# Kernel optimization log

Measured on AMD Instinct MI355X. Metric: run time of the kernel, lower is better.

## Reference

```python
import jax, jax.numpy as jnp
import numpy as np
from jax import lax

T, N, E = 12, 10000, 160000
C_IN, C_H, C_OUT = 32, 64, 32
EPS = 1e-5


def _glorot(key, shape):
    fan_in, fan_out = shape[-2] if len(shape) > 1 else shape[0], shape[-1]
    s = (6.0 / (fan_in + fan_out)) ** 0.5
    return jax.random.uniform(key, shape, jnp.float32, -s, s)


def setup_inputs() -> dict:
    key = jax.random.key(0)
    ks = jax.random.split(key, 16)
    inp = {
        "x": jax.random.normal(ks[0], (T, N, C_IN), jnp.float32),
        "edge_index": jax.random.randint(ks[1], (2, E), 0, N, jnp.int32),
        "edge_weight": jax.random.uniform(ks[2], (E,), jnp.float32),
        # layer 1 (input layer): in=C_IN -> C_H
        "conv_w1": _glorot(ks[3], (C_H, C_IN, 3)) * 0.1,
        "conv_b1": jnp.zeros((C_H,), jnp.float32),
        "gamma1": jnp.ones((C_H,), jnp.float32),
        "beta1": jnp.zeros((C_H,), jnp.float32),
        "gcn_w1": _glorot(ks[4], (C_H, C_H)),
        "gcn_b1": jnp.zeros((C_H,), jnp.float32),
        # layer 2 (hidden layer): C_H -> C_H
        "conv_w2": _glorot(ks[5], (C_H, C_H, 3)) * 0.1,
        "conv_b2": jnp.zeros((C_H,), jnp.float32),
        "gamma2": jnp.ones((C_H,), jnp.float32),
        "beta2": jnp.zeros((C_H,), jnp.float32),
        "gcn_w2": _glorot(ks[6], (C_H, C_H)),
        "gcn_b2": jnp.zeros((C_H,), jnp.float32),
        # output linear: C_H -> C_OUT
        "out_w": _glorot(ks[7], (C_H, C_OUT)),
        "out_b": jnp.zeros((C_OUT,), jnp.float32),
    }
    return inp


def _stgcn_layer(x, edge_index, edge_weight, cw, cb, gamma, beta, gw, gb):
    # x: [T, N, C_in]  ->  torch.stack(x).permute(1,2,0) = [N, C_in, T]
    xs = jnp.transpose(x, (1, 2, 0))
    h = lax.conv_general_dilated(xs, cw, (1,), [(1, 1)],
                                 dimension_numbers=("NCH", "OIH", "NCH"))
    h = h + cb[None, :, None]
    # InstanceNorm1d(affine) over the temporal dim
    mu = h.mean(-1, keepdims=True)
    var = ((h - mu) ** 2).mean(-1, keepdims=True)
    h = (h - mu) * lax.rsqrt(var + EPS) * gamma[None, :, None] + beta[None, :, None]
    h = jax.nn.relu(h)
    h = jnp.transpose(h, (2, 0, 1))  # [T, N, C_out]
    # GCNConv per timestep (vectorized over T)
    src, dst = edge_index[0], edge_index[1]
    n = h.shape[1]
    deg = jnp.zeros((n,), h.dtype).at[dst].add(edge_weight) + 1.0  # self-loop weight 1
    dis = lax.rsqrt(deg)
    norm = dis[src] * edge_weight * dis[dst]  # [E]
    xw = jnp.einsum("tnc,cd->tnd", h, gw)  # [T, N, C_out]
    msg = xw[:, src, :] * norm[None, :, None]  # [T, E, C_out]
    agg = jax.vmap(lambda m: jax.ops.segment_sum(m, dst, num_segments=n))(msg)
    agg = agg + (dis * dis)[None, :, None] * xw + gb  # self loop + bias
    return agg


def reference(x, edge_index, edge_weight,
              conv_w1, conv_b1, gamma1, beta1, gcn_w1, gcn_b1,
              conv_w2, conv_b2, gamma2, beta2, gcn_w2, gcn_b2,
              out_w, out_b):
    h = _stgcn_layer(x, edge_index, edge_weight,
                     conv_w1, conv_b1, gamma1, beta1, gcn_w1, gcn_b1)
    h = _stgcn_layer(h, edge_index, edge_weight,
                     conv_w2, conv_b2, gamma2, beta2, gcn_w2, gcn_b2)
    out = jnp.einsum("tnc,co->tno", h, out_w) + out_b  # per-t linear
    return out.mean(axis=0)  # [N, C_OUT]
```

## Files before the change

kernel.cpp:

```cpp
#include <hip/hip_runtime.h>
#include <hip/hip_bf16.h>
#include <stdint.h>

#define MAXDEG 64

typedef short s16x8 __attribute__((ext_vector_type(8)));
typedef short s16x4 __attribute__((ext_vector_type(4)));
typedef float f32x4 __attribute__((ext_vector_type(4)));

static __device__ __forceinline__ float us2f(unsigned short u) {
    union { float f; unsigned int i; } cv; cv.i = ((unsigned int)u) << 16; return cv.f;
}
static __device__ __forceinline__ unsigned short f2us(float f) {
    __hip_bfloat16 h = __float2bfloat16(f);
    return *(unsigned short*)&h;
}

__global__ void k_build_ell(const int* __restrict__ ei, const float* __restrict__ ew,
                            float* __restrict__ deg, unsigned* __restrict__ cnt,
                            int2* __restrict__ ell, int E)
{
    int e = blockIdx.x * 256 + threadIdx.x;
    if (e >= E) return;
    int s = ei[e], d = ei[E + e];
    float w = ew[e];
    atomicAdd(&deg[d], w);
    unsigned slot = atomicAdd(&cnt[d], 1u);
    if (slot < MAXDEG) ell[(size_t)d * MAXDEG + slot] = make_int2(s, __float_as_int(w));
}

__global__ void k_norm(int2* __restrict__ ell, const unsigned* __restrict__ cnt,
                       const float* __restrict__ deg, int N)
{
    int idx = blockIdx.x * 256 + threadIdx.x;
    if (idx >= N * MAXDEG) return;
    int n = idx >> 6;
    int s = idx & (MAXDEG - 1);
    unsigned dg = cnt[n]; if (dg > MAXDEG) dg = MAXDEG;
    if ((unsigned)s >= dg) return;
    int2 p = ell[idx];
    unsigned sx = (unsigned)p.x;
    float nrm = (sx < (unsigned)N)
        ? rsqrtf(deg[sx] + 1.0f) * __int_as_float(p.y) * rsqrtf(deg[n] + 1.0f) : 0.f;
    ell[idx] = make_int2(p.x, __float_as_int(nrm));
}

#define ACCE(NRM, V0, V1, V2)                                                          \
    a[0] = fmaf(NRM, us2f(V0.x), a[0]);  a[1] = fmaf(NRM, us2f(V0.y), a[1]);           \
    a[2] = fmaf(NRM, us2f(V0.z), a[2]);  a[3] = fmaf(NRM, us2f(V0.w), a[3]);           \
    a[4] = fmaf(NRM, us2f(V1.x), a[4]);  a[5] = fmaf(NRM, us2f(V1.y), a[5]);           \
    a[6] = fmaf(NRM, us2f(V1.z), a[6]);  a[7] = fmaf(NRM, us2f(V1.w), a[7]);           \
    a[8] = fmaf(NRM, us2f(V2.x), a[8]);  a[9] = fmaf(NRM, us2f(V2.y), a[9]);           \
    a[10] = fmaf(NRM, us2f(V2.z), a[10]); a[11] = fmaf(NRM, us2f(V2.w), a[11]);

#define EDGE_GATHER(P)                                                      \
    {                                                                       \
        unsigned sx = (unsigned)(P).x;                                      \
        if (sx >= (unsigned)N) sx = 0;          \
        float nrm = __int_as_float((P).y);                                  \
        const unsigned short* qp = xw_in + (size_t)sx * 768 + L * 4;        \
        ushort4 w0 = *(const ushort4*)qp;                                   \
        ushort4 w1 = *(const ushort4*)(qp + 256);                           \
        ushort4 w2 = *(const ushort4*)(qp + 512);                           \
        ACCE(nrm, w0, w1, w2)                                               \
    }

template<int CIN>
__global__ __launch_bounds__(512, 4) void k_layer_a(
    const float* __restrict__ x_in,
    const float* __restrict__ cw,
    const float* __restrict__ gm, const float* __restrict__ bt,
    const float* __restrict__ gw,
    unsigned short* __restrict__ xw_out, int N)
{
    constexpr int KT   = CIN / 32;
    constexpr int WSTR = (CIN == 64) ? 72 : 40;
    __shared__ __align__(16) short WT[3 * 64 * WSTR];
    __shared__ __align__(16) short gwT[64 * 72];
    __shared__ __align__(16) short xh[8][14 * 72];

    const int tid = threadIdx.x;
    const int nn = tid >> 6;
    const int c = tid & 63;
    const int m = c & 15;
    const int q = c >> 4;
    const int mrow = (m < 12) ? m : 11;
    int n = blockIdx.x * 8 + nn;
    if (n >= N) n = N - 1;

    for (int g = tid; g < 3 * 64 * CIN; g += 512) {
        int kk = g / (64 * CIN);
        int r = g - kk * 64 * CIN;
        int cc = r / CIN, ci = r - cc * CIN;
        WT[kk * (64 * WSTR) + cc * WSTR + ci] = (short)f2us(cw[(cc * CIN + ci) * 3 + kk]);
    }
    for (int g = tid; g < 4096; g += 512) {
        int cc = g >> 6, d = g & 63;
        gwT[d * 72 + cc] = (short)f2us(gw[g]);
    }
    #pragma unroll
    for (int it = 0; it < (12 * CIN) / 64; ++it) {
        int i = it * 64 + c;
        int t = i / CIN, ci = i - t * CIN;
        xh[nn][(t + 1) * 72 + ci] = (short)f2us(x_in[((size_t)t * N + n) * CIN + ci]);
    }
    if (c < CIN) { xh[nn][c] = 0; xh[nn][13 * 72 + c] = 0; }
    __syncthreads();

    f32x4 acc[4];
    #pragma unroll
    for (int nt = 0; nt < 4; ++nt) acc[nt] = (f32x4){0.f, 0.f, 0.f, 0.f};
    #pragma unroll
    for (int kk = 0; kk < 3; ++kk) {
        #pragma unroll
        for (int kt = 0; kt < KT; ++kt) {
            s16x8 aA = *(const s16x8*)&xh[nn][(mrow + kk) * 72 + kt * 32 + q * 8];
            #pragma unroll
            for (int nt = 0; nt < 4; ++nt) {
                s16x8 bB = *(const s16x8*)&WT[kk * (64 * WSTR) + (nt * 16 + m) * WSTR + kt * 32 + q * 8];
                acc[nt] = __builtin_amdgcn_mfma_f32_16x16x32_bf16(aA, bB, acc[nt], 0, 0, 0);
            }
        }
    }

    #pragma unroll
    for (int nt = 0; nt < 4; ++nt) {
        float s  = acc[nt][0] + acc[nt][1] + acc[nt][2] + acc[nt][3];
        float s2 = acc[nt][0] * acc[nt][0] + acc[nt][1] * acc[nt][1]
                 + acc[nt][2] * acc[nt][2] + acc[nt][3] * acc[nt][3];
        if (q == 3) { s = 0.f; s2 = 0.f; }
        s  += __shfl_xor(s, 16);  s  += __shfl_xor(s, 32);
        s2 += __shfl_xor(s2, 16); s2 += __shfl_xor(s2, 32);
        const float mu  = s * (1.f / 12.f);
        const float var = s2 * (1.f / 12.f) - mu * mu;
        const float scn = rsqrtf(var + 1e-5f) * gm[nt * 16 + m];
        const float sbn = bt[nt * 16 + m];
        if (q < 3) {
            #pragma unroll
            for (int reg = 0; reg < 4; ++reg) {
                float h = fmaf(acc[nt][reg] - mu, scn, sbn);
                h = h > 0.f ? h : 0.f;
                xh[nn][(q * 4 + reg) * 72 + nt * 16 + m] = (short)f2us(h);
            }
        }
    }

    s16x8 a2[2];
    #pragma unroll
    for (int kt2 = 0; kt2 < 2; ++kt2)
        a2[kt2] = *(const s16x8*)&xh[nn][mrow * 72 + kt2 * 32 + q * 8];
    f32x4 acc2[4];
    #pragma unroll
    for (int nt = 0; nt < 4; ++nt) acc2[nt] = (f32x4){0.f, 0.f, 0.f, 0.f};
    #pragma unroll
    for (int nt = 0; nt < 4; ++nt) {
        #pragma unroll
        for (int kt2 = 0; kt2 < 2; ++kt2) {
            s16x8 b2 = *(const s16x8*)&gwT[(nt * 16 + m) * 72 + kt2 * 32 + q * 8];
            acc2[nt] = __builtin_amdgcn_mfma_f32_16x16x32_bf16(a2[kt2], b2, acc2[nt], 0, 0, 0);
        }
    }

    unsigned short* dst = xw_out + (size_t)n * 768;
    if (q < 3) {
        #pragma unroll
        for (int nt = 0; nt < 4; ++nt)
            #pragma unroll
            for (int reg = 0; reg < 4; ++reg)
                dst[(q * 4 + reg) * 64 + nt * 16 + m] = f2us(acc2[nt][reg]);
    }
}

__global__ __launch_bounds__(512, 4) void k_gather_a(
    const unsigned short* __restrict__ xw_in,
    const int2* __restrict__ ell, const unsigned* __restrict__ cnt,
    const float* __restrict__ deg, const float* __restrict__ gb,
    const float* __restrict__ cw,
    const float* __restrict__ gm, const float* __restrict__ bt,
    const float* __restrict__ gw,
    unsigned short* __restrict__ rowmean, int N)
{
    constexpr int WSTR = 72;
    __shared__ __align__(16) short WT[3 * 64 * WSTR];
    __shared__ __align__(16) short gwT[64 * 72];
    __shared__ __align__(16) short xh[8][14 * 72];

    const int tid = threadIdx.x;
    const int nn = tid >> 6;
    const int L = tid & 63;
    const int m = L & 15;
    const int q = L >> 4;
    const int mrow = (m < 12) ? m : 11;
    int n = blockIdx.x * 8 + nn;
    if (n >= N) n = N - 1;

    for (int g = tid; g < 3 * 64 * 64; g += 512) {
        int kk = g >> 12;
        int r = g & 4095;
        int cc = r >> 6, ci = r & 63;
        WT[kk * (64 * WSTR) + cc * WSTR + ci] = (short)f2us(cw[(cc * 64 + ci) * 3 + kk]);
    }
    for (int g = tid; g < 4096; g += 512) {
        int cc = g >> 6, d = g & 63;
        gwT[d * 72 + cc] = (short)f2us(gw[g]);
    }
    xh[nn][L] = 0; xh[nn][13 * 72 + L] = 0;
    __syncthreads();

    const float dn = rsqrtf(deg[n] + 1.0f);
    const float d2 = dn * dn;
    float a[12];
    {
        const unsigned short* self = xw_in + (size_t)n * 768 + L * 4;
        ushort4 v0 = *(const ushort4*)self;
        ushort4 v1 = *(const ushort4*)(self + 256);
        ushort4 v2 = *(const ushort4*)(self + 512);
        const int c0 = (L * 4) & 63;
        const float g0 = gb[c0], g1 = gb[c0 + 1], g2 = gb[c0 + 2], g3 = gb[c0 + 3];
        a[0] = fmaf(d2, us2f(v0.x), g0); a[1] = fmaf(d2, us2f(v0.y), g1);
        a[2] = fmaf(d2, us2f(v0.z), g2); a[3] = fmaf(d2, us2f(v0.w), g3);
        a[4] = fmaf(d2, us2f(v1.x), g0); a[5] = fmaf(d2, us2f(v1.y), g1);
        a[6] = fmaf(d2, us2f(v1.z), g2); a[7] = fmaf(d2, us2f(v1.w), g3);
        a[8] = fmaf(d2, us2f(v2.x), g0); a[9] = fmaf(d2, us2f(v2.y), g1);
        a[10] = fmaf(d2, us2f(v2.z), g2); a[11] = fmaf(d2, us2f(v2.w), g3);
    }
    unsigned dg = cnt[n]; if (dg > MAXDEG) dg = MAXDEG;
    const int2* row = ell + (size_t)n * MAXDEG;
    unsigned e = 0;
    for (; e + 4 <= dg; e += 4) {
        int2 p0 = row[e], p1 = row[e + 1], p2 = row[e + 2], p3 = row[e + 3];
        EDGE_GATHER(p0) EDGE_GATHER(p1) EDGE_GATHER(p2) EDGE_GATHER(p3)
    }
    for (; e < dg; ++e) { int2 p0 = row[e]; EDGE_GATHER(p0) }

    #pragma unroll
    for (int j = 0; j < 3; ++j) {
        s16x4 s4 = { (short)f2us(a[j * 4 + 0]), (short)f2us(a[j * 4 + 1]),
                     (short)f2us(a[j * 4 + 2]), (short)f2us(a[j * 4 + 3]) };
        *(s16x4*)&xh[nn][(j * 4 + q + 1) * 72 + ((L * 4) & 63)] = s4;
    }

    f32x4 acc[4];
    #pragma unroll
    for (int nt = 0; nt < 4; ++nt) acc[nt] = (f32x4){0.f, 0.f, 0.f, 0.f};
    #pragma unroll
    for (int kk = 0; kk < 3; ++kk) {
        #pragma unroll
        for (int kt = 0; kt < 2; ++kt) {
            s16x8 aA = *(const s16x8*)&xh[nn][(mrow + kk) * 72 + kt * 32 + q * 8];
            #pragma unroll
            for (int nt = 0; nt < 4; ++nt) {
                s16x8 bB = *(const s16x8*)&WT[kk * (64 * WSTR) + (nt * 16 + m) * WSTR + kt * 32 + q * 8];
                acc[nt] = __builtin_amdgcn_mfma_f32_16x16x32_bf16(aA, bB, acc[nt], 0, 0, 0);
            }
        }
    }

    #pragma unroll
    for (int nt = 0; nt < 4; ++nt) {
        float s  = acc[nt][0] + acc[nt][1] + acc[nt][2] + acc[nt][3];
        float s2 = acc[nt][0] * acc[nt][0] + acc[nt][1] * acc[nt][1]
                 + acc[nt][2] * acc[nt][2] + acc[nt][3] * acc[nt][3];
        if (q == 3) { s = 0.f; s2 = 0.f; }
        s  += __shfl_xor(s, 16);  s  += __shfl_xor(s, 32);
        s2 += __shfl_xor(s2, 16); s2 += __shfl_xor(s2, 32);
        const float mu  = s * (1.f / 12.f);
        const float var = s2 * (1.f / 12.f) - mu * mu;
        const float scn = rsqrtf(var + 1e-5f) * gm[nt * 16 + m];
        const float sbn = bt[nt * 16 + m];
        if (q < 3) {
            #pragma unroll
            for (int reg = 0; reg < 4; ++reg) {
                float h = fmaf(acc[nt][reg] - mu, scn, sbn);
                h = h > 0.f ? h : 0.f;
                xh[nn][(q * 4 + reg) * 72 + nt * 16 + m] = (short)f2us(h);
            }
        }
    }

    s16x8 a2[2];
    #pragma unroll
    for (int kt2 = 0; kt2 < 2; ++kt2)
        a2[kt2] = *(const s16x8*)&xh[nn][mrow * 72 + kt2 * 32 + q * 8];
    f32x4 acc2[4];
    #pragma unroll
    for (int nt = 0; nt < 4; ++nt) acc2[nt] = (f32x4){0.f, 0.f, 0.f, 0.f};
    #pragma unroll
    for (int nt = 0; nt < 4; ++nt) {
        #pragma unroll
        for (int kt2 = 0; kt2 < 2; ++kt2) {
            s16x8 b2 = *(const s16x8*)&gwT[(nt * 16 + m) * 72 + kt2 * 32 + q * 8];
            acc2[nt] = __builtin_amdgcn_mfma_f32_16x16x32_bf16(a2[kt2], b2, acc2[nt], 0, 0, 0);
        }
    }

    #pragma unroll
    for (int nt = 0; nt < 4; ++nt) {
        float pm = (q < 3) ? (acc2[nt][0] + acc2[nt][1] + acc2[nt][2] + acc2[nt][3]) : 0.f;
        pm += __shfl_xor(pm, 16); pm += __shfl_xor(pm, 32);
        if (q == 0)
            rowmean[(size_t)n * 64 + nt * 16 + m] = f2us(pm * (1.f / 12.f));
    }
}

__global__ __launch_bounds__(256) void k_final(
    const unsigned short* __restrict__ rowmean, const int2* __restrict__ ell,
    const unsigned* __restrict__ cnt, const float* __restrict__ deg,
    const float* __restrict__ gb,
    const float* __restrict__ ow, const float* __restrict__ ob,
    float* __restrict__ dout, int N)
{
    __shared__ __align__(16) float hbuf[4][64];
    const int tid = threadIdx.x;
    const int nn = tid >> 6, L = tid & 63;
    int n = blockIdx.x * 4 + nn;
    if (n >= N) n = N - 1;
    const float dn = rsqrtf(deg[n] + 1.0f);
    const float d2 = dn * dn;

    float a = fmaf(d2, us2f(rowmean[(size_t)n * 64 + L]), gb[L]);

    unsigned dg = cnt[n]; if (dg > MAXDEG) dg = MAXDEG;
    const int2* row = ell + (size_t)n * MAXDEG;
    unsigned e = 0;
    for (; e + 8 <= dg; e += 8) {
        #pragma unroll
        for (int i = 0; i < 8; ++i) {
            int2 p = row[e + i];
            unsigned sx = (unsigned)p.x;
            if (sx >= (unsigned)N) sx = 0;
            a = fmaf(__int_as_float(p.y), us2f(rowmean[(size_t)sx * 64 + L]), a);
        }
    }
    for (; e < dg; ++e) {
        int2 p = row[e];
        unsigned sx = (unsigned)p.x;
        if (sx >= (unsigned)N) sx = 0;
        a = fmaf(__int_as_float(p.y), us2f(rowmean[(size_t)sx * 64 + L]), a);
    }

    hbuf[nn][L] = a;
    __syncthreads();
    if (L < 32) {
        float oa = ob[L];
        #pragma unroll
        for (int cc = 0; cc < 64; ++cc)
            oa = fmaf(hbuf[nn][cc], ow[cc * 32 + L], oa);
        dout[(size_t)n * 32 + L] = oa;
    }
}

extern "C" void kernel_launch(void* const* d_in, const int* in_sizes, int n_in,
                              void* d_out, int out_size, void* d_ws, size_t ws_size,
                              hipStream_t stream)
{
    const float* x   = (const float*)d_in[0];
    const int*   ei  = (const int*)d_in[1];
    const float* ew  = (const float*)d_in[2];
    const float* cw1 = (const float*)d_in[3];
    const float* gm1 = (const float*)d_in[5];
    const float* bt1 = (const float*)d_in[6];
    const float* gw1 = (const float*)d_in[7];
    const float* gb1 = (const float*)d_in[8];
    const float* cw2 = (const float*)d_in[9];
    const float* gm2 = (const float*)d_in[11];
    const float* bt2 = (const float*)d_in[12];
    const float* gw2 = (const float*)d_in[13];
    const float* gb2 = (const float*)d_in[14];
    const float* ow  = (const float*)d_in[15];
    const float* ob  = (const float*)d_in[16];

    const int N = in_sizes[0] / (12 * 32);
    const int E = in_sizes[2];

    char* p0 = (char*)d_ws;
    char* p = p0;
    float* deg = (float*)p;          p += (size_t)N * 4;
    unsigned* cnt = (unsigned*)p;    p += (size_t)N * 4;
    p = (char*)(((uintptr_t)p + 255) & ~(uintptr_t)255);
    int2* ell = (int2*)p;            p += (size_t)N * MAXDEG * 8;
    p = (char*)(((uintptr_t)p + 255) & ~(uintptr_t)255);
    unsigned short* bufXW1 = (unsigned short*)p; p += (size_t)N * 768 * 2;
    unsigned short* rowmean = (unsigned short*)p; p += (size_t)N * 64 * 2;

    const size_t need = (size_t)(p - p0);
    if (ws_size < need) {
        hipMemsetAsync(d_out, 0, (size_t)out_size * 4, stream);
        return;
    }

    hipMemsetAsync(deg, 0, (size_t)N * 8, stream);

    const int eb  = (E + 255) / 256;
    const int nb8 = (N + 7) / 8;
    const int nb4 = (N + 3) / 4;
    k_build_ell<<<eb, 256, 0, stream>>>(ei, ew, deg, cnt, ell, E);
    k_norm<<<(N * MAXDEG + 255) / 256, 256, 0, stream>>>(ell, cnt, deg, N);

    k_layer_a<32><<<nb8, 512, 0, stream>>>(x, cw1, gm1, bt1, gw1, bufXW1, N);
    k_gather_a<<<nb8, 512, 0, stream>>>(bufXW1, ell, cnt, deg, gb1,
                                        cw2, gm2, bt2, gw2, rowmean, N);
    k_final<<<nb4, 256, 0, stream>>>(rowmean, ell, cnt, deg, gb2, ow, ob, (float*)d_out, N);
}
```

Measured before the change: 194.0 us.

## Use persistent blocks with atomic work-stealing for layer and gather kernels

Converts k_layer_a and k_gather_a into persistent kernels with a fixed grid (1024 and 768 blocks). Each wavefront takes node indices from a global atomic counter and loops until all nodes are done. This amortizes the per-block staging of conv and GCN weights into shared memory over many nodes and balances the uneven per-node degree work in the gather. The cost is one atomic per node per wavefront and two counters zeroed by the existing memset.

Measured after the change: 543.3 us. +180.1%, slower.

```diff
diff --git a/kernel.cpp b/kernel.cpp
--- a/kernel.cpp
+++ b/kernel.cpp
@@ -71,7 +71,7 @@
     const float* __restrict__ cw,
     const float* __restrict__ gm, const float* __restrict__ bt,
     const float* __restrict__ gw,
-    unsigned short* __restrict__ xw_out, int N)
+    unsigned short* __restrict__ xw_out, unsigned* __restrict__ ctr, int N)
 {
     constexpr int KT   = CIN / 32;
     constexpr int WSTR = (CIN == 64) ? 72 : 40;
@@ -85,8 +85,6 @@
     const int m = c & 15;
     const int q = c >> 4;
     const int mrow = (m < 12) ? m : 11;
-    int n = blockIdx.x * 8 + nn;
-    if (n >= N) n = N - 1;
 
     for (int g = tid; g < 3 * 64 * CIN; g += 512) {
         int kk = g / (64 * CIN);
@@ -98,76 +96,85 @@
         int cc = g >> 6, d = g & 63;
         gwT[d * 72 + cc] = (short)f2us(gw[g]);
     }
-    #pragma unroll
-    for (int it = 0; it < (12 * CIN) / 64; ++it) {
-        int i = it * 64 + c;
-        int t = i / CIN, ci = i - t * CIN;
-        xh[nn][(t + 1) * 72 + ci] = (short)f2us(x_in[((size_t)t * N + n) * CIN + ci]);
-    }
-    if (c < CIN) { xh[nn][c] = 0; xh[nn][13 * 72 + c] = 0; }
+    if (c < CIN) xh[nn][13 * 72 + c] = 0;
     __syncthreads();
 
-    f32x4 acc[4];
-    #pragma unroll
-    for (int nt = 0; nt < 4; ++nt) acc[nt] = (f32x4){0.f, 0.f, 0.f, 0.f};
-    #pragma unroll
-    for (int kk = 0; kk < 3; ++kk) {
-        #pragma unroll
-        for (int kt = 0; kt < KT; ++kt) {
-            s16x8 aA = *(const s16x8*)&xh[nn][(mrow + kk) * 72 + kt * 32 + q * 8];
+    for (;;) {
+        unsigned n;
+        if (c == 0) n = atomicAdd(ctr, 1u);
+        n = (unsigned)__shfl((int)n, 0);
+        if (n >= (unsigned)N) break;
+
+        if (c < CIN) xh[nn][c] = 0;
+        #pragma unroll
+        for (int it = 0; it < (12 * CIN) / 64; ++it) {
+            int i = it * 64 + c;
+            int t = i / CIN, ci = i - t * CIN;
+            xh[nn][(t + 1) * 72 + ci] = (short)f2us(x_in[((size_t)t * N + n) * CIN + ci]);
+        }
+
+        f32x4 acc[4];
+        #pragma unroll
+        for (int nt = 0; nt < 4; ++nt) acc[nt] = (f32x4){0.f, 0.f, 0.f, 0.f};
+        #pragma unroll
+        for (int kk = 0; kk < 3; ++kk) {
             #pragma unroll
-            for (int nt = 0; nt < 4; ++nt) {
-                s16x8 bB = *(const s16x8*)&WT[kk * (64 * WSTR) + (nt * 16 + m) * WSTR + kt * 32 + q * 8];
-                acc[nt] = __builtin_amdgcn_mfma_f32_16x16x32_bf16(aA, bB, acc[nt], 0, 0, 0);
-            }
-        }
-    }
-
-    #pragma unroll
-    for (int nt = 0; nt < 4; ++nt) {
-        float s  = acc[nt][0] + acc[nt][1] + acc[nt][2] + acc[nt][3];
-        float s2 = acc[nt][0] * acc[nt][0] + acc[nt][1] * acc[nt][1]
-                 + acc[nt][2] * acc[nt][2] + acc[nt][3] * acc[nt][3];
-        if (q == 3) { s = 0.f; s2 = 0.f; }
-        s  += __shfl_xor(s, 16);  s  += __shfl_xor(s, 32);
-        s2 += __shfl_xor(s2, 16); s2 += __shfl_xor(s2, 32);
-        const float mu  = s * (1.f / 12.f);
-        const float var = s2 * (1.f / 12.f) - mu * mu;
-        const float scn = rsqrtf(var + 1e-5f) * gm[nt * 16 + m];
-        const float sbn = bt[nt * 16 + m];
+            for (int kt = 0; kt < KT; ++kt) {
+                s16x8 aA = *(const s16x8*)&xh[nn][(mrow + kk) * 72 + kt * 32 + q * 8];
+                #pragma unroll
+                for (int nt = 0; nt < 4; ++nt) {
+                    s16x8 bB = *(const s16x8*)&WT[kk * (64 * WSTR) + (nt * 16 + m) * WSTR + kt * 32 + q * 8];
+                    acc[nt] = __builtin_amdgcn_mfma_f32_16x16x32_bf16(aA, bB, acc[nt], 0, 0, 0);
+                }
+            }
+        }
+
+        #pragma unroll
+        for (int nt = 0; nt < 4; ++nt) {
+            float s  = acc[nt][0] + acc[nt][1] + acc[nt][2] + acc[nt][3];
+            float s2 = acc[nt][0] * acc[nt][0] + acc[nt][1] * acc[nt][1]
+                     + acc[nt][2] * acc[nt][2] + acc[nt][3] * acc[nt][3];
+            if (q == 3) { s = 0.f; s2 = 0.f; }
+            s  += __shfl_xor(s, 16);  s  += __shfl_xor(s, 32);
+            s2 += __shfl_xor(s2, 16); s2 += __shfl_xor(s2, 32);
+            const float mu  = s * (1.f / 12.f);
+            const float var = s2 * (1.f / 12.f) - mu * mu;
+            const float scn = rsqrtf(var + 1e-5f) * gm[nt * 16 + m];
+            const float sbn = bt[nt * 16 + m];
+            if (q < 3) {
+                #pragma unroll
+                for (int reg = 0; reg < 4; ++reg) {
+                    float h = fmaf(acc[nt][reg] - mu, scn, sbn);
+                    h = h > 0.f ? h : 0.f;
+                    xh[nn][(q * 4 + reg) * 72 + nt * 16 + m] = (short)f2us(h);
+                }
+            }
+        }
+
+        s16x8 a2[2];
+        #pragma unroll
+        for (int kt2 = 0; kt2 < 2; ++kt2)
+            a2[kt2] = *(const s16x8*)&xh[nn][mrow * 72 + kt2 * 32 + q * 8];
+        f32x4 acc2[4];
+        #pragma unroll
+        for (int nt = 0; nt < 4; ++nt) acc2[nt] = (f32x4){0.f, 0.f, 0.f, 0.f};
+        #pragma unroll
+        for (int nt = 0; nt < 4; ++nt) {
+            #pragma unroll
+            for (int kt2 = 0; kt2 < 2; ++kt2) {
+                s16x8 b2 = *(const s16x8*)&gwT[(nt * 16 + m) * 72 + kt2 * 32 + q * 8];
+                acc2[nt] = __builtin_amdgcn_mfma_f32_16x16x32_bf16(a2[kt2], b2, acc2[nt], 0, 0, 0);
+            }
+        }
+
+        unsigned short* dst = xw_out + (size_t)n * 768;
         if (q < 3) {
             #pragma unroll
-            for (int reg = 0; reg < 4; ++reg) {
-                float h = fmaf(acc[nt][reg] - mu, scn, sbn);
-                h = h > 0.f ? h : 0.f;
-                xh[nn][(q * 4 + reg) * 72 + nt * 16 + m] = (short)f2us(h);
-            }
-        }
-    }
-
-    s16x8 a2[2];
-    #pragma unroll
-    for (int kt2 = 0; kt2 < 2; ++kt2)
-        a2[kt2] = *(const s16x8*)&xh[nn][mrow * 72 + kt2 * 32 + q * 8];
-    f32x4 acc2[4];
-    #pragma unroll
-    for (int nt = 0; nt < 4; ++nt) acc2[nt] = (f32x4){0.f, 0.f, 0.f, 0.f};
-    #pragma unroll
-    for (int nt = 0; nt < 4; ++nt) {
-        #pragma unroll
-        for (int kt2 = 0; kt2 < 2; ++kt2) {
-            s16x8 b2 = *(const s16x8*)&gwT[(nt * 16 + m) * 72 + kt2 * 32 + q * 8];
-            acc2[nt] = __builtin_amdgcn_mfma_f32_16x16x32_bf16(a2[kt2], b2, acc2[nt], 0, 0, 0);
-        }
-    }
-
-    unsigned short* dst = xw_out + (size_t)n * 768;
-    if (q < 3) {
-        #pragma unroll
-        for (int nt = 0; nt < 4; ++nt)
-            #pragma unroll
-            for (int reg = 0; reg < 4; ++reg)
-                dst[(q * 4 + reg) * 64 + nt * 16 + m] = f2us(acc2[nt][reg]);
+            for (int nt = 0; nt < 4; ++nt)
+                #pragma unroll
+                for (int reg = 0; reg < 4; ++reg)
+                    dst[(q * 4 + reg) * 64 + nt * 16 + m] = f2us(acc2[nt][reg]);
+        }
     }
 }
 
@@ -178,7 +185,7 @@
     const float* __restrict__ cw,
     const float* __restrict__ gm, const float* __restrict__ bt,
     const float* __restrict__ gw,
-    unsigned short* __restrict__ rowmean, int N)
+    unsigned short* __restrict__ rowmean, unsigned* __restrict__ ctr, int N)
 {
     constexpr int WSTR = 72;
     __shared__ __align__(16) short WT[3 * 64 * WSTR];
@@ -191,8 +198,6 @@
     const int m = L & 15;
     const int q = L >> 4;
     const int mrow = (m < 12) ? m : 11;
-    int n = blockIdx.x * 8 + nn;
-    if (n >= N) n = N - 1;
 
     for (int g = tid; g < 3 * 64 * 64; g += 512) {
         int kk = g >> 12;
@@ -204,102 +209,110 @@
         int cc = g >> 6, d = g & 63;
         gwT[d * 72 + cc] = (short)f2us(gw[g]);
     }
-    xh[nn][L] = 0; xh[nn][13 * 72 + L] = 0;
+    xh[nn][13 * 72 + L] = 0;
     __syncthreads();
 
-    const float dn = rsqrtf(deg[n] + 1.0f);
-    const float d2 = dn * dn;
-    float a[12];
-    {
-        const unsigned short* self = xw_in + (size_t)n * 768 + L * 4;
-        ushort4 v0 = *(const ushort4*)self;
-        ushort4 v1 = *(const ushort4*)(self + 256);
-        ushort4 v2 = *(const ushort4*)(self + 512);
-        const int c0 = (L * 4) & 63;
-        const float g0 = gb[c0], g1 = gb[c0 + 1], g2 = gb[c0 + 2], g3 = gb[c0 + 3];
-        a[0] = fmaf(d2, us2f(v0.x), g0); a[1] = fmaf(d2, us2f(v0.y), g1);
-        a[2] = fmaf(d2, us2f(v0.z), g2); a[3] = fmaf(d2, us2f(v0.w), g3);
-        a[4] = fmaf(d2, us2f(v1.x), g0); a[5] = fmaf(d2, us2f(v1.y), g1);
-        a[6] = fmaf(d2, us2f(v1.z), g2); a[7] = fmaf(d2, us2f(v1.w), g3);
-        a[8] = fmaf(d2, us2f(v2.x), g0); a[9] = fmaf(d2, us2f(v2.y), g1);
-        a[10] = fmaf(d2, us2f(v2.z), g2); a[11] = fmaf(d2, us2f(v2.w), g3);
-    }
-    unsigned dg = cnt[n]; if (dg > MAXDEG) dg = MAXDEG;
-    const int2* row = ell + (size_t)n * MAXDEG;
-    unsigned e = 0;
-    for (; e + 4 <= dg; e += 4) {
-        int2 p0 = row[e], p1 = row[e + 1], p2 = row[e + 2], p3 = row[e + 3];
-        EDGE_GATHER(p0) EDGE_GATHER(p1) EDGE_GATHER(p2) EDGE_GATHER(p3)
-    }
-    for (; e < dg; ++e) { int2 p0 = row[e]; EDGE_GATHER(p0) }
-
-    #pragma unroll
-    for (int j = 0; j < 3; ++j) {
-        s16x4 s4 = { (short)f2us(a[j * 4 + 0]), (short)f2us(a[j * 4 + 1]),
-                     (short)f2us(a[j * 4 + 2]), (short)f2us(a[j * 4 + 3]) };
-        *(s16x4*)&xh[nn][(j * 4 + q + 1) * 72 + ((L * 4) & 63)] = s4;
-    }
-
-    f32x4 acc[4];
-    #pragma unroll
-    for (int nt = 0; nt < 4; ++nt) acc[nt] = (f32x4){0.f, 0.f, 0.f, 0.f};
-    #pragma unroll
-    for (int kk = 0; kk < 3; ++kk) {
-        #pragma unroll
-        for (int kt = 0; kt < 2; ++kt) {
-            s16x8 aA = *(const s16x8*)&xh[nn][(mrow + kk) * 72 + kt * 32 + q * 8];
+    for (;;) {
+        unsigned n;
+        if (L == 0) n = atomicAdd(ctr, 1u);
+        n = (unsigned)__shfl((int)n, 0);
+        if (n >= (unsigned)N) break;
+
+        const float dn = rsqrtf(deg[n] + 1.0f);
+        const float d2 = dn * dn;
+        float a[12];
+        {
+            const unsigned short* self = xw_in + (size_t)n * 768 + L * 4;
+            ushort4 v0 = *(const ushort4*)self;
+            ushort4 v1 = *(const ushort4*)(self + 256);
+            ushort4 v2 = *(const ushort4*)(self + 512);
+            const int c0 = (L * 4) & 63;
+            const float g0 = gb[c0], g1 = gb[c0 + 1], g2 = gb[c0 + 2], g3 = gb[c0 + 3];
+            a[0] = fmaf(d2, us2f(v0.x), g0); a[1] = fmaf(d2, us2f(v0.y), g1);
+            a[2] = fmaf(d2, us2f(v0.z), g2); a[3] = fmaf(d2, us2f(v0.w), g3);
+            a[4] = fmaf(d2, us2f(v1.x), g0); a[5] = fmaf(d2, us2f(v1.y), g1);
+            a[6] = fmaf(d2, us2f(v1.z), g2); a[7] = fmaf(d2, us2f(v1.w), g3);
+            a[8] = fmaf(d2, us2f(v2.x), g0); a[9] = fmaf(d2, us2f(v2.y), g1);
+            a[10] = fmaf(d2, us2f(v2.z), g2); a[11] = fmaf(d2, us2f(v2.w), g3);
+        }
+        unsigned dg = cnt[n]; if (dg > MAXDEG) dg = MAXDEG;
+        const int2* row = ell + (size_t)n * MAXDEG;
+        unsigned e = 0;
+        for (; e + 4 <= dg; e += 4) {
+            int2 p0 = row[e], p1 = row[e + 1], p2 = row[e + 2], p3 = row[e + 3];
+            EDGE_GATHER(p0) EDGE_GATHER(p1) EDGE_GATHER(p2) EDGE_GATHER(p3)
+        }
+        for (; e < dg; ++e) { int2 p0 = row[e]; EDGE_GATHER(p0) }
+
+        xh[nn][L] = 0;
+        #pragma unroll
+        for (int j = 0; j < 3; ++j) {
+            s16x4 s4 = { (short)f2us(a[j * 4 + 0]), (short)f2us(a[j * 4 + 1]),
+                         (short)f2us(a[j * 4 + 2]), (short)f2us(a[j * 4 + 3]) };
+            *(s16x4*)&xh[nn][(j * 4 + q + 1) * 72 + ((L * 4) & 63)] = s4;
+        }
+
+        f32x4 acc[4];
+        #pragma unroll
+        for (int nt = 0; nt < 4; ++nt) acc[nt] = (f32x4){0.f, 0.f, 0.f, 0.f};
+        #pragma unroll
+        for (int kk = 0; kk < 3; ++kk) {
             #pragma unroll
-            for (int nt = 0; nt < 4; ++nt) {
-                s16x8 bB = *(const s16x8*)&WT[kk * (64 * WSTR) + (nt * 16 + m) * WSTR + kt * 32 + q * 8];
-                acc[nt] = __builtin_amdgcn_mfma_f32_16x16x32_bf16(aA, bB, acc[nt], 0, 0, 0);
-            }
-        }
-    }
-
-    #pragma unroll
-    for (int nt = 0; nt < 4; ++nt) {
-        float s  = acc[nt][0] + acc[nt][1] + acc[nt][2] + acc[nt][3];
-        float s2 = acc[nt][0] * acc[nt][0] + acc[nt][1] * acc[nt][1]
-                 + acc[nt][2] * acc[nt][2] + acc[nt][3] * acc[nt][3];
-        if (q == 3) { s = 0.f; s2 = 0.f; }
-        s  += __shfl_xor(s, 16);  s  += __shfl_xor(s, 32);
-        s2 += __shfl_xor(s2, 16); s2 += __shfl_xor(s2, 32);
-        const float mu  = s * (1.f / 12.f);
-        const float var = s2 * (1.f / 12.f) - mu * mu;
-        const float scn = rsqrtf(var + 1e-5f) * gm[nt * 16 + m];
-        const float sbn = bt[nt * 16 + m];
-        if (q < 3) {
+            for (int kt = 0; kt < 2; ++kt) {
+                s16x8 aA = *(const s16x8*)&xh[nn][(mrow + kk) * 72 + kt * 32 + q * 8];
+                #pragma unroll
+                for (int nt = 0; nt < 4; ++nt) {
+                    s16x8 bB = *(const s16x8*)&WT[kk * (64 * WSTR) + (nt * 16 + m) * WSTR + kt * 32 + q * 8];
+                    acc[nt] = __builtin_amdgcn_mfma_f32_16x16x32_bf16(aA, bB, acc[nt], 0, 0, 0);
+                }
+            }
+        }
+
+        #pragma unroll
+        for (int nt = 0; nt < 4; ++nt) {
+            float s  = acc[nt][0] + acc[nt][1] + acc[nt][2] + acc[nt][3];
+            float s2 = acc[nt][0] * acc[nt][0] + acc[nt][1] * acc[nt][1]
+                     + acc[nt][2] * acc[nt][2] + acc[nt][3] * acc[nt][3];
+            if (q == 3) { s = 0.f; s2 = 0.f; }
+            s  += __shfl_xor(s, 16);  s  += __shfl_xor(s, 32);
+            s2 += __shfl_xor(s2, 16); s2 += __shfl_xor(s2, 32);
+            const float mu  = s * (1.f / 12.f);
+            const float var = s2 * (1.f / 12.f) - mu * mu;
+            const float scn = rsqrtf(var + 1e-5f) * gm[nt * 16 + m];
+            const float sbn = bt[nt * 16 + m];
+            if (q < 3) {
+                #pragma unroll
+                for (int reg = 0; reg < 4; ++reg) {
+                    float h = fmaf(acc[nt][reg] - mu, scn, sbn);
+                    h = h > 0.f ? h : 0.f;
+                    xh[nn][(q * 4 + reg) * 72 + nt * 16 + m] = (short)f2us(h);
+                }
+            }
+        }
+
+        s16x8 a2[2];
+        #pragma unroll
+        for (int kt2 = 0; kt2 < 2; ++kt2)
+            a2[kt2] = *(const s16x8*)&xh[nn][mrow * 72 + kt2 * 32 + q * 8];
+        f32x4 acc2[4];
+        #pragma unroll
+        for (int nt = 0; nt < 4; ++nt) acc2[nt] = (f32x4){0.f, 0.f, 0.f, 0.f};
+        #pragma unroll
+        for (int nt = 0; nt < 4; ++nt) {
             #pragma unroll
-            for (int reg = 0; reg < 4; ++reg) {
-                float h = fmaf(acc[nt][reg] - mu, scn, sbn);
-                h = h > 0.f ? h : 0.f;
-                xh[nn][(q * 4 + reg) * 72 + nt * 16 + m] = (short)f2us(h);
-            }
-        }
-    }
-
-    s16x8 a2[2];
-    #pragma unroll
-    for (int kt2 = 0; kt2 < 2; ++kt2)
-        a2[kt2] = *(const s16x8*)&xh[nn][mrow * 72 + kt2 * 32 + q * 8];
-    f32x4 acc2[4];
-    #pragma unroll
-    for (int nt = 0; nt < 4; ++nt) acc2[nt] = (f32x4){0.f, 0.f, 0.f, 0.f};
-    #pragma unroll
-    for (int nt = 0; nt < 4; ++nt) {
-        #pragma unroll
-        for (int kt2 = 0; kt2 < 2; ++kt2) {
-            s16x8 b2 = *(const s16x8*)&gwT[(nt * 16 + m) * 72 + kt2 * 32 + q * 8];
-            acc2[nt] = __builtin_amdgcn_mfma_f32_16x16x32_bf16(a2[kt2], b2, acc2[nt], 0, 0, 0);
-        }
-    }
-
-    #pragma unroll
-    for (int nt = 0; nt < 4; ++nt) {
-        float pm = (q < 3) ? (acc2[nt][0] + acc2[nt][1] + acc2[nt][2] + acc2[nt][3]) : 0.f;
-        pm += __shfl_xor(pm, 16); pm += __shfl_xor(pm, 32);
-        if (q == 0)
-            rowmean[(size_t)n * 64 + nt * 16 + m] = f2us(pm * (1.f / 12.f));
+            for (int kt2 = 0; kt2 < 2; ++kt2) {
+                s16x8 b2 = *(const s16x8*)&gwT[(nt * 16 + m) * 72 + kt2 * 32 + q * 8];
+                acc2[nt] = __builtin_amdgcn_mfma_f32_16x16x32_bf16(a2[kt2], b2, acc2[nt], 0, 0, 0);
+            }
+        }
+
+        #pragma unroll
+        for (int nt = 0; nt < 4; ++nt) {
+            float pm = (q < 3) ? (acc2[nt][0] + acc2[nt][1] + acc2[nt][2] + acc2[nt][3]) : 0.f;
+            pm += __shfl_xor(pm, 16); pm += __shfl_xor(pm, 32);
+            if (q == 0)
+                rowmean[(size_t)n * 64 + nt * 16 + m] = f2us(pm * (1.f / 12.f));
+        }
     }
 }
 
@@ -374,7 +387,9 @@
     const int E = in_sizes[2];
 
     char* p0 = (char*)d_ws;
-    char* p = p0;
+    unsigned* ctrA = (unsigned*)p0;
+    unsigned* ctrG = (unsigned*)(p0 + 4);
+    char* p = p0 + 256;
     float* deg = (float*)p;          p += (size_t)N * 4;
     unsigned* cnt = (unsigned*)p;    p += (size_t)N * 4;
     p = (char*)(((uintptr_t)p + 255) & ~(uintptr_t)255);
@@ -389,16 +404,15 @@
         return;
     }
 
-    hipMemsetAsync(deg, 0, (size_t)N * 8, stream);
+    hipMemsetAsync(p0, 0, 256 + (size_t)N * 8, stream);
 
     const int eb  = (E + 255) / 256;
-    const int nb8 = (N + 7) / 8;
     const int nb4 = (N + 3) / 4;
     k_build_ell<<<eb, 256, 0, stream>>>(ei, ew, deg, cnt, ell, E);
     k_norm<<<(N * MAXDEG + 255) / 256, 256, 0, stream>>>(ell, cnt, deg, N);
 
-    k_layer_a<32><<<nb8, 512, 0, stream>>>(x, cw1, gm1, bt1, gw1, bufXW1, N);
-    k_gather_a<<<nb8, 512, 0, stream>>>(bufXW1, ell, cnt, deg, gb1,
-                                        cw2, gm2, bt2, gw2, rowmean, N);
+    k_layer_a<32><<<1024, 512, 0, stream>>>(x, cw1, gm1, bt1, gw1, bufXW1, ctrA, N);
+    k_gather_a<<<768, 512, 0, stream>>>(bufXW1, ell, cnt, deg, gb1,
+                                        cw2, gm2, bt2, gw2, rowmean, ctrG, N);
     k_final<<<nb4, 256, 0, stream>>>(rowmean, ell, cnt, deg, gb2, ow, ob, (float*)d_out, N);
 }
```

## Process two nodes per wave in gather kernel with padded ELL rows

Applied to the files above, without the earlier changes.

k_gather_a now handles two nodes per wavefront, so it launches half as many blocks. This halves the per-block cost of converting and staging the conv and GCN weights into LDS. The edge loops of the two nodes are interleaved to keep more independent gathers in flight. k_norm now fills every unused ELL slot with (index 0, weight 0), which lets the gather loops run to the larger of the two degrees and drops the source-index bounds checks in both gather kernels. In exchange, each wave does wasted zero-weight loads for the lower-degree node and holds two sets of accumulators, which raises register pressure.

Measured after the change: 196.7 us. About the same (+1.4%).

```diff
diff --git a/kernel.cpp b/kernel.cpp
--- a/kernel.cpp
+++ b/kernel.cpp
@@ -37,33 +37,31 @@
     int n = idx >> 6;
     int s = idx & (MAXDEG - 1);
     unsigned dg = cnt[n]; if (dg > MAXDEG) dg = MAXDEG;
-    if ((unsigned)s >= dg) return;
-    int2 p = ell[idx];
-    unsigned sx = (unsigned)p.x;
-    float nrm = (sx < (unsigned)N)
-        ? rsqrtf(deg[sx] + 1.0f) * __int_as_float(p.y) * rsqrtf(deg[n] + 1.0f) : 0.f;
-    ell[idx] = make_int2(p.x, __float_as_int(nrm));
-}
-
-#define ACCE(NRM, V0, V1, V2)                                                          \
-    a[0] = fmaf(NRM, us2f(V0.x), a[0]);  a[1] = fmaf(NRM, us2f(V0.y), a[1]);           \
-    a[2] = fmaf(NRM, us2f(V0.z), a[2]);  a[3] = fmaf(NRM, us2f(V0.w), a[3]);           \
-    a[4] = fmaf(NRM, us2f(V1.x), a[4]);  a[5] = fmaf(NRM, us2f(V1.y), a[5]);           \
-    a[6] = fmaf(NRM, us2f(V1.z), a[6]);  a[7] = fmaf(NRM, us2f(V1.w), a[7]);           \
-    a[8] = fmaf(NRM, us2f(V2.x), a[8]);  a[9] = fmaf(NRM, us2f(V2.y), a[9]);           \
-    a[10] = fmaf(NRM, us2f(V2.z), a[10]); a[11] = fmaf(NRM, us2f(V2.w), a[11]);
-
-#define EDGE_GATHER(P)                                                      \
-    {                                                                       \
-        unsigned sx = (unsigned)(P).x;                                      \
-        if (sx >= (unsigned)N) sx = 0;          \
-        float nrm = __int_as_float((P).y);                                  \
-        const unsigned short* qp = xw_in + (size_t)sx * 768 + L * 4;        \
-        ushort4 w0 = *(const ushort4*)qp;                                   \
-        ushort4 w1 = *(const ushort4*)(qp + 256);                           \
-        ushort4 w2 = *(const ushort4*)(qp + 512);                           \
-        ACCE(nrm, w0, w1, w2)                                               \
-    }
+    int sxo = 0; float nrm = 0.f;
+    if ((unsigned)s < dg) {
+        int2 p = ell[idx];
+        unsigned sx = (unsigned)p.x;
+        if (sx < (unsigned)N) {
+            nrm = rsqrtf(deg[sx] + 1.0f) * __int_as_float(p.y) * rsqrtf(deg[n] + 1.0f);
+            sxo = p.x;
+        }
+    }
+    ell[idx] = make_int2(sxo, __float_as_int(nrm));
+}
+
+static __device__ __forceinline__ void edge_acc(float* __restrict__ a, float nrm,
+                                                const unsigned short* __restrict__ qp)
+{
+    ushort4 w0 = *(const ushort4*)qp;
+    ushort4 w1 = *(const ushort4*)(qp + 256);
+    ushort4 w2 = *(const ushort4*)(qp + 512);
+    a[0] = fmaf(nrm, us2f(w0.x), a[0]);  a[1] = fmaf(nrm, us2f(w0.y), a[1]);
+    a[2] = fmaf(nrm, us2f(w0.z), a[2]);  a[3] = fmaf(nrm, us2f(w0.w), a[3]);
+    a[4] = fmaf(nrm, us2f(w1.x), a[4]);  a[5] = fmaf(nrm, us2f(w1.y), a[5]);
+    a[6] = fmaf(nrm, us2f(w1.z), a[6]);  a[7] = fmaf(nrm, us2f(w1.w), a[7]);
+    a[8] = fmaf(nrm, us2f(w2.x), a[8]);  a[9] = fmaf(nrm, us2f(w2.y), a[9]);
+    a[10] = fmaf(nrm, us2f(w2.z), a[10]); a[11] = fmaf(nrm, us2f(w2.w), a[11]);
+}
 
 template<int CIN>
 __global__ __launch_bounds__(512, 4) void k_layer_a(
@@ -191,8 +189,6 @@
     const int m = L & 15;
     const int q = L >> 4;
     const int mrow = (m < 12) ? m : 11;
-    int n = blockIdx.x * 8 + nn;
-    if (n >= N) n = N - 1;
 
     for (int g = tid; g < 3 * 64 * 64; g += 512) {
         int kk = g >> 12;
@@ -204,19 +200,27 @@
         int cc = g >> 6, d = g & 63;
         gwT[d * 72 + cc] = (short)f2us(gw[g]);
     }
-    xh[nn][L] = 0; xh[nn][13 * 72 + L] = 0;
+    xh[nn][13 * 72 + L] = 0;
     __syncthreads();
 
-    const float dn = rsqrtf(deg[n] + 1.0f);
-    const float d2 = dn * dn;
-    float a[12];
-    {
+    int base = blockIdx.x * 16 + nn * 2;
+    unsigned nP[2];
+    nP[0] = (unsigned)((base     < N) ? base     : N - 1);
+    nP[1] = (unsigned)((base + 1 < N) ? base + 1 : N - 1);
+
+    float aP[2][12];
+    #pragma unroll
+    for (int j = 0; j < 2; ++j) {
+        const unsigned n = nP[j];
+        const float dn = rsqrtf(deg[n] + 1.0f);
+        const float d2 = dn * dn;
         const unsigned short* self = xw_in + (size_t)n * 768 + L * 4;
         ushort4 v0 = *(const ushort4*)self;
         ushort4 v1 = *(const ushort4*)(self + 256);
         ushort4 v2 = *(const ushort4*)(self + 512);
         const int c0 = (L * 4) & 63;
         const float g0 = gb[c0], g1 = gb[c0 + 1], g2 = gb[c0 + 2], g3 = gb[c0 + 3];
+        float* a = aP[j];
         a[0] = fmaf(d2, us2f(v0.x), g0); a[1] = fmaf(d2, us2f(v0.y), g1);
         a[2] = fmaf(d2, us2f(v0.z), g2); a[3] = fmaf(d2, us2f(v0.w), g3);
         a[4] = fmaf(d2, us2f(v1.x), g0); a[5] = fmaf(d2, us2f(v1.y), g1);
@@ -224,82 +228,101 @@
         a[8] = fmaf(d2, us2f(v2.x), g0); a[9] = fmaf(d2, us2f(v2.y), g1);
         a[10] = fmaf(d2, us2f(v2.z), g2); a[11] = fmaf(d2, us2f(v2.w), g3);
     }
-    unsigned dg = cnt[n]; if (dg > MAXDEG) dg = MAXDEG;
-    const int2* row = ell + (size_t)n * MAXDEG;
-    unsigned e = 0;
-    for (; e + 4 <= dg; e += 4) {
-        int2 p0 = row[e], p1 = row[e + 1], p2 = row[e + 2], p3 = row[e + 3];
-        EDGE_GATHER(p0) EDGE_GATHER(p1) EDGE_GATHER(p2) EDGE_GATHER(p3)
-    }
-    for (; e < dg; ++e) { int2 p0 = row[e]; EDGE_GATHER(p0) }
-
-    #pragma unroll
-    for (int j = 0; j < 3; ++j) {
-        s16x4 s4 = { (short)f2us(a[j * 4 + 0]), (short)f2us(a[j * 4 + 1]),
-                     (short)f2us(a[j * 4 + 2]), (short)f2us(a[j * 4 + 3]) };
-        *(s16x4*)&xh[nn][(j * 4 + q + 1) * 72 + ((L * 4) & 63)] = s4;
-    }
-
-    f32x4 acc[4];
-    #pragma unroll
-    for (int nt = 0; nt < 4; ++nt) acc[nt] = (f32x4){0.f, 0.f, 0.f, 0.f};
-    #pragma unroll
-    for (int kk = 0; kk < 3; ++kk) {
-        #pragma unroll
-        for (int kt = 0; kt < 2; ++kt) {
-            s16x8 aA = *(const s16x8*)&xh[nn][(mrow + kk) * 72 + kt * 32 + q * 8];
+    {
+        unsigned dg0 = cnt[nP[0]]; if (dg0 > MAXDEG) dg0 = MAXDEG;
+        unsigned dg1 = cnt[nP[1]]; if (dg1 > MAXDEG) dg1 = MAXDEG;
+        unsigned dgm = dg0 > dg1 ? dg0 : dg1;
+        const int2* r0 = ell + (size_t)nP[0] * MAXDEG;
+        const int2* r1 = ell + (size_t)nP[1] * MAXDEG;
+        unsigned e = 0;
+        for (; e + 2 <= dgm; e += 2) {
+            int2 p00 = r0[e], p01 = r0[e + 1], p10 = r1[e], p11 = r1[e + 1];
+            edge_acc(aP[0], __int_as_float(p00.y), xw_in + (size_t)(unsigned)p00.x * 768 + L * 4);
+            edge_acc(aP[1], __int_as_float(p10.y), xw_in + (size_t)(unsigned)p10.x * 768 + L * 4);
+            edge_acc(aP[0], __int_as_float(p01.y), xw_in + (size_t)(unsigned)p01.x * 768 + L * 4);
+            edge_acc(aP[1], __int_as_float(p11.y), xw_in + (size_t)(unsigned)p11.x * 768 + L * 4);
+        }
+        if (e < dgm) {
+            int2 p00 = r0[e], p10 = r1[e];
+            edge_acc(aP[0], __int_as_float(p00.y), xw_in + (size_t)(unsigned)p00.x * 768 + L * 4);
+            edge_acc(aP[1], __int_as_float(p10.y), xw_in + (size_t)(unsigned)p10.x * 768 + L * 4);
+        }
+    }
+
+    #pragma unroll
+    for (int j = 0; j < 2; ++j) {
+        const unsigned n = nP[j];
+        const float* a = aP[j];
+
+        xh[nn][L] = 0;
+        #pragma unroll
+        for (int j3 = 0; j3 < 3; ++j3) {
+            s16x4 s4 = { (short)f2us(a[j3 * 4 + 0]), (short)f2us(a[j3 * 4 + 1]),
+                         (short)f2us(a[j3 * 4 + 2]), (short)f2us(a[j3 * 4 + 3]) };
+            *(s16x4*)&xh[nn][(j3 * 4 + q + 1) * 72 + ((L * 4) & 63)] = s4;
+        }
+
+        f32x4 acc[4];
+        #pragma unroll
+        for (int nt = 0; nt < 4; ++nt) acc[nt] = (f32x4){0.f, 0.f, 0.f, 0.f};
+        #pragma unroll
+        for (int kk = 0; kk < 3; ++kk) {
             #pragma unroll
-            for (int nt = 0; nt < 4; ++nt) {
-                s16x8 bB = *(const s16x8*)&WT[kk * (64 * WSTR) + (nt * 16 + m) * WSTR + kt * 32 + q * 8];
-                acc[nt] = __builtin_amdgcn_mfma_f32_16x16x32_bf16(aA, bB, acc[nt], 0, 0, 0);
+            for (int kt = 0; kt < 2; ++kt) {
+                s16x8 aA = *(const s16x8*)&xh[nn][(mrow + kk) * 72 + kt * 32 + q * 8];
+                #pragma unroll
+                for (int nt = 0; nt < 4; ++nt) {
+                    s16x8 bB = *(const s16x8*)&WT[kk * (64 * WSTR) + (nt * 16 + m) * WSTR + kt * 32 + q * 8];
+                    acc[nt] = __builtin_amdgcn_mfma_f32_16x16x32_bf16(aA, bB, acc[nt], 0, 0, 0);
+                }
             }
         }
-    }
-
-    #pragma unroll
-    for (int nt = 0; nt < 4; ++nt) {
-        float s  = acc[nt][0] + acc[nt][1] + acc[nt][2] + acc[nt][3];
-        float s2 = acc[nt][0] * acc[nt][0] + acc[nt][1] * acc[nt][1]
-                 + acc[nt][2] * acc[nt][2] + acc[nt][3] * acc[nt][3];
-        if (q == 3) { s = 0.f; s2 = 0.f; }
-        s  += __shfl_xor(s, 16);  s  += __shfl_xor(s, 32);
-        s2 += __shfl_xor(s2, 16); s2 += __shfl_xor(s2, 32);
-        const float mu  = s * (1.f / 12.f);
-        const float var = s2 * (1.f / 12.f) - mu * mu;
-        const float scn = rsqrtf(var + 1e-5f) * gm[nt * 16 + m];
-        const float sbn = bt[nt * 16 + m];
-        if (q < 3) {
+
+        #pragma unroll
+        for (int nt = 0; nt < 4; ++nt) {
+            float s  = acc[nt][0] + acc[nt][1] + acc[nt][2] + acc[nt][3];
+            float s2 = acc[nt][0] * acc[nt][0] + acc[nt][1] * acc[nt][1]
+                     + acc[nt][2] * acc[nt][2] + acc[nt][3] * acc[nt][3];
+            if (q == 3) { s = 0.f; s2 = 0.f; }
+            s  += __shfl_xor(s, 16);  s  += __shfl_xor(s, 32);
+            s2 += __shfl_xor(s2, 16); s2 += __shfl_xor(s2, 32);
+            const float mu  = s * (1.f / 12.f);
+            const float var = s2 * (1.f / 12.f) - mu * mu;
+            const float scn = rsqrtf(var + 1e-5f) * gm[nt * 16 + m];
+            const float sbn = bt[nt * 16 + m];
+            if (q < 3) {
+                #pragma unroll
+                for (int reg = 0; reg < 4; ++reg) {
+                    float h = fmaf(acc[nt][reg] - mu, scn, sbn);
+                    h = h > 0.f ? h : 0.f;
+                    xh[nn][(q * 4 + reg) * 72 + nt * 16 + m] = (short)f2us(h);
+                }
+            }
+        }
+
+        s16x8 a2[2];
+        #pragma unroll
+        for (int kt2 = 0; kt2 < 2; ++kt2)
+            a2[kt2] = *(const s16x8*)&xh[nn][mrow * 72 + kt2 * 32 + q * 8];
+        f32x4 acc2[4];
+        #pragma unroll
+        for (int nt = 0; nt < 4; ++nt) acc2[nt] = (f32x4){0.f, 0.f, 0.f, 0.f};
+        #pragma unroll
+        for (int nt = 0; nt < 4; ++nt) {
             #pragma unroll
-            for (int reg = 0; reg < 4; ++reg) {
-                float h = fmaf(acc[nt][reg] - mu, scn, sbn);
-                h = h > 0.f ? h : 0.f;
-                xh[nn][(q * 4 + reg) * 72 + nt * 16 + m] = (short)f2us(h);
+            for (int kt2 = 0; kt2 < 2; ++kt2) {
+                s16x8 b2 = *(const s16x8*)&gwT[(nt * 16 + m) * 72 + kt2 * 32 + q * 8];
+                acc2[nt] = __builtin_amdgcn_mfma_f32_16x16x32_bf16(a2[kt2], b2, acc2[nt], 0, 0, 0);
             }
         }
-    }
-
-    s16x8 a2[2];
-    #pragma unroll
-    for (int kt2 = 0; kt2 < 2; ++kt2)
-        a2[kt2] = *(const s16x8*)&xh[nn][mrow * 72 + kt2 * 32 + q * 8];
-    f32x4 acc2[4];
-    #pragma unroll
-    for (int nt = 0; nt < 4; ++nt) acc2[nt] = (f32x4){0.f, 0.f, 0.f, 0.f};
-    #pragma unroll
-    for (int nt = 0; nt < 4; ++nt) {
-        #pragma unroll
-        for (int kt2 = 0; kt2 < 2; ++kt2) {
-            s16x8 b2 = *(const s16x8*)&gwT[(nt * 16 + m) * 72 + kt2 * 32 + q * 8];
-            acc2[nt] = __builtin_amdgcn_mfma_f32_16x16x32_bf16(a2[kt2], b2, acc2[nt], 0, 0, 0);
-        }
-    }
-
-    #pragma unroll
-    for (int nt = 0; nt < 4; ++nt) {
-        float pm = (q < 3) ? (acc2[nt][0] + acc2[nt][1] + acc2[nt][2] + acc2[nt][3]) : 0.f;
-        pm += __shfl_xor(pm, 16); pm += __shfl_xor(pm, 32);
-        if (q == 0)
-            rowmean[(size_t)n * 64 + nt * 16 + m] = f2us(pm * (1.f / 12.f));
+
+        #pragma unroll
+        for (int nt = 0; nt < 4; ++nt) {
+            float pm = (q < 3) ? (acc2[nt][0] + acc2[nt][1] + acc2[nt][2] + acc2[nt][3]) : 0.f;
+            pm += __shfl_xor(pm, 16); pm += __shfl_xor(pm, 32);
+            if (q == 0)
+                rowmean[(size_t)n * 64 + nt * 16 + m] = f2us(pm * (1.f / 12.f));
+        }
     }
 }
 
@@ -327,16 +350,12 @@
         #pragma unroll
         for (int i = 0; i < 8; ++i) {
             int2 p = row[e + i];
-            unsigned sx = (unsigned)p.x;
-            if (sx >= (unsigned)N) sx = 0;
-            a = fmaf(__int_as_float(p.y), us2f(rowmean[(size_t)sx * 64 + L]), a);
+            a = fmaf(__int_as_float(p.y), us2f(rowmean[(size_t)(unsigned)p.x * 64 + L]), a);
         }
     }
     for (; e < dg; ++e) {
         int2 p = row[e];
-        unsigned sx = (unsigned)p.x;
-        if (sx >= (unsigned)N) sx = 0;
-        a = fmaf(__int_as_float(p.y), us2f(rowmean[(size_t)sx * 64 + L]), a);
+        a = fmaf(__int_as_float(p.y), us2f(rowmean[(size_t)(unsigned)p.x * 64 + L]), a);
     }
 
     hbuf[nn][L] = a;
@@ -391,14 +410,15 @@
 
     hipMemsetAsync(deg, 0, (size_t)N * 8, stream);
 
-    const int eb  = (E + 255) / 256;
-    const int nb8 = (N + 7) / 8;
-    const int nb4 = (N + 3) / 4;
+    const int eb   = (E + 255) / 256;
+    const int nb8  = (N + 7) / 8;
+    const int nb16 = (N + 15) / 16;
+    const int nb4  = (N + 3) / 4;
     k_build_ell<<<eb, 256, 0, stream>>>(ei, ew, deg, cnt, ell, E);
     k_norm<<<(N * MAXDEG + 255) / 256, 256, 0, stream>>>(ell, cnt, deg, N);
 
     k_layer_a<32><<<nb8, 512, 0, stream>>>(x, cw1, gm1, bt1, gw1, bufXW1, N);
-    k_gather_a<<<nb8, 512, 0, stream>>>(bufXW1, ell, cnt, deg, gb1,
-                                        cw2, gm2, bt2, gw2, rowmean, N);
+    k_gather_a<<<nb16, 512, 0, stream>>>(bufXW1, ell, cnt, deg, gb1,
+                                         cw2, gm2, bt2, gw2, rowmean, N);
     k_final<<<nb4, 256, 0, stream>>>(rowmean, ell, cnt, deg, gb2, ow, ob, (float*)d_out, N);
 }
```
